# Kernel optimization log

Measured on AMD Instinct MI355X. Metric: run time of the kernel, lower is better.

Reference implementation:

```python
import jax, jax.numpy as jnp
import numpy as np

B, S, H, R, IN, OPS, NPAD = 128, 128, 512, 16, 2, 5, 16
L = IN + NPAD
NEG = -1e12


def setup_inputs():
    key = jax.random.key(0)
    ks = jax.random.split(key, 32)
    def n(k, shape, scale=1.0):
        return jax.random.normal(k, shape, jnp.float32) * scale
    s = 0.05
    return {
        "encoder_outputs": n(ks[0], (S, B, H)),
        "current_emb": n(ks[1], (B, 1, H)),
        "left_childs": n(ks[2], (B, H)),
        "padding_hidden": jnp.zeros((1, H), jnp.float32),
        "num_pades": n(ks[3], (B, NPAD, H)),
        "rule_scores": n(ks[4], (R, H)),
        "embedding_weight": n(ks[5], (1, IN, H)),
        "W_concat_l": n(ks[6], (H, H), s), "b_concat_l": jnp.zeros((H,)),
        "W_concat_lg": n(ks[7], (H, H), s), "b_concat_lg": jnp.zeros((H,)),
        "W_concat_r": n(ks[8], (2 * H, H), s), "b_concat_r": jnp.zeros((H,)),
        "W_concat_rg": n(ks[9], (2 * H, H), s), "b_concat_rg": jnp.zeros((H,)),
        "W_tree_attn": n(ks[10], (2 * H, H), s), "b_tree_attn": jnp.zeros((H,)),
        "W_tree_score": n(ks[11], (H, 1), s), "b_tree_score": jnp.zeros((1,)),
        "W_rule_attn": n(ks[12], (2 * H, H), s), "b_rule_attn": jnp.zeros((H,)),
        "W_rule_score": n(ks[13], (H, 1), s), "b_rule_score": jnp.zeros((1,)),
        "W_rp1": n(ks[14], (H, H), s), "b_rp1": jnp.zeros((H,)),
        "W_rp2": n(ks[15], (H, 1), s), "b_rp2": jnp.zeros((1,)),
        "W_sc_attn": n(ks[16], (3 * H, H), s), "b_sc_attn": jnp.zeros((H,)),
        "W_sc_score": n(ks[17], (H, 1), s),
        "W_ops": n(ks[18], (2 * H, OPS), s), "b_ops": jnp.zeros((OPS,)),
        "seq_mask": jax.random.randint(ks[19], (B, S), 0, 2).astype(jnp.int32),
        "mask_nums": jax.random.randint(ks[20], (B, L), 0, 2).astype(jnp.int32),
        "has_left": jax.random.randint(ks[21], (B,), 0, 2).astype(jnp.int32),
        "stack_empty": jax.random.randint(ks[22], (B,), 0, 2).astype(jnp.int32),
    }


def reference(encoder_outputs, current_emb, left_childs, padding_hidden, num_pades,
              rule_scores, embedding_weight,
              W_concat_l, b_concat_l, W_concat_lg, b_concat_lg,
              W_concat_r, b_concat_r, W_concat_rg, b_concat_rg,
              W_tree_attn, b_tree_attn, W_tree_score, b_tree_score,
              W_rule_attn, b_rule_attn, W_rule_score, b_rule_score,
              W_rp1, b_rp1, W_rp2, b_rp2,
              W_sc_attn, b_sc_attn, W_sc_score, W_ops, b_ops,
              seq_mask, mask_nums, has_left, stack_empty):
    sm = seq_mask.astype(bool)          # [B,S] True = pad
    nm = mask_nums.astype(bool)         # [B,L]
    hl = has_left.astype(bool)[:, None]
    se = stack_empty.astype(bool)[:, None]
    h = encoder_outputs.shape[-1]
    # gather top-of-stack embedding, padding for empty stacks (the ragged python loop)
    c = jnp.where(se, padding_hidden[0], current_emb[:, 0])  # [B,H]
    # gated combine: left_child==None branch vs cat(left, c) branch (dropout=eval)
    node_l = jnp.tanh(c @ W_concat_l + b_concat_l) * jax.nn.sigmoid(c @ W_concat_lg + b_concat_lg)
    node_r = (jnp.tanh(left_childs @ W_concat_r[:h] + c @ W_concat_r[h:] + b_concat_r)
              * jax.nn.sigmoid(left_childs @ W_concat_rg[:h] + c @ W_concat_rg[h:] + b_concat_rg))
    q = jnp.where(hl, node_r, node_l)                        # [B,H]
    current_node = q[:, None, :]                              # [B,1,H]
    # TreeAttn: concat(hidden, enc) -> Linear -> tanh -> Linear(H,1) -> softmax over S
    e = jnp.tanh(q @ W_tree_attn[:h] + encoder_outputs @ W_tree_attn[h:] + b_tree_attn)  # [S,B,H]
    ae = (e @ W_tree_score)[..., 0] + b_tree_score[0]         # [S,B]
    ae = jnp.where(sm, NEG, ae.T)                             # [B,S]
    current_attn = jax.nn.softmax(ae, axis=1)                 # [B,S]
    current_context = jnp.einsum('bs,sbh->bh', current_attn, encoder_outputs)[:, None, :]
    # RuleAttn: concat(enc, rule) additive attention, softmax over S
    re = jnp.tanh(encoder_outputs @ W_rule_attn[:h]
                  + (rule_scores @ W_rule_attn[h:])[:, None, None, :]
                  + b_rule_attn)                              # [R,S,B,H]
    r_ae = (re @ W_rule_score)[..., 0] + b_rule_score[0]      # [R,S,B]
    r_ae = jnp.transpose(r_ae, (2, 0, 1))                     # [B,R,S]
    r_ae = jnp.where(sm[:, None, :], NEG, r_ae)
    rules_attn = jax.nn.softmax(r_ae, axis=-1)
    rules_context = jnp.einsum('brs,sbh->brh', rules_attn + 0.2 * current_attn[:, None, :], encoder_outputs)
    rule_prob = jax.nn.softmax((jnp.tanh(rules_context @ W_rp1 + b_rp1) @ W_rp2)[..., 0] + b_rp2[0], axis=-1)  # [B,R]
    # leaf scoring: Score(cat(node, context), [const_embs | num_pades])
    bsz = q.shape[0]
    ew = jnp.concatenate([jnp.broadcast_to(embedding_weight, (bsz,) + embedding_weight.shape[1:]), num_pades], axis=1)  # [B,L,H]
    leaf = jnp.concatenate([q, current_context[:, 0]], axis=1)  # [B,2H]
    sc = jnp.tanh((leaf @ W_sc_attn[:2 * h])[:, None, :] + ew @ W_sc_attn[2 * h:] + b_sc_attn)  # [B,L,H]
    num_score = jnp.where(nm, NEG, (sc @ W_sc_score)[..., 0])   # [B,L]
    op = leaf @ W_ops + b_ops                                   # [B,OPS]
    return num_score, op, current_node, current_context, ew, rule_prob
```

## Files before the change

kernel.cpp:

```cpp
#include <hip/hip_runtime.h>
#include <hip/hip_bf16.h>

#define B_ 128
#define S_ 128
#define H_ 512
#define R_ 16
#define IN_ 2
#define OPS_ 5
#define NPAD_ 16
#define L_ 18
#define NEGV (-1000000000000.0f)
#define C2_ (-2.885390081777927f)

typedef __bf16 bf16_t;
typedef bf16_t bf16x8 __attribute__((ext_vector_type(8)));
typedef float floatx4 __attribute__((ext_vector_type(4)));

__device__ __forceinline__ float rcp_f(float x) { return __builtin_amdgcn_rcpf(x); }
__device__ __forceinline__ float exp2_f(float x) { return __builtin_amdgcn_exp2f(x); }

__device__ __forceinline__ float fast_tanh(float x) {
    return 2.0f * rcp_f(1.0f + exp2_f(C2_ * x)) - 1.0f;
}
__device__ __forceinline__ float fast_sigmoid(float x) {
    return rcp_f(1.0f + exp2_f(-1.4426950408889634f * x));
}
__device__ __forceinline__ unsigned short f2bf(float f) {
    unsigned int u = __builtin_bit_cast(unsigned int, f);
    u += 0x7fff + ((u >> 16) & 1);
    return (unsigned short)(u >> 16);
}
__device__ __forceinline__ float bf2f(unsigned short u) {
    return __builtin_bit_cast(float, (unsigned int)u << 16);
}

#define LSTR 40

__device__ __forceinline__ void mfma_tile(const unsigned short* __restrict__ A,
                                          const unsigned short* __restrict__ Bt,
                                          void* __restrict__ Cv, bool bf16_out,
                                          int m0, int n0, int K, int ldc,
                                          unsigned short* As, unsigned short* Bs) {
    const int tid  = threadIdx.x;
    const int wid  = tid >> 6, lane = tid & 63;
    const int quad = lane >> 4, mn = lane & 15;
    const int wm = (wid & 1) * 64, wn = (wid >> 1) * 64;
    const int sr = tid >> 2;
    const int sc = (tid & 3) * 8;

    floatx4 acc[4][4] = {};

    for (int k0 = 0; k0 < K; k0 += 32) {
        uint4 a0 = *(const uint4*)(A  + (size_t)(m0 + sr)      * K + k0 + sc);
        uint4 a1 = *(const uint4*)(A  + (size_t)(m0 + sr + 64) * K + k0 + sc);
        uint4 b0 = *(const uint4*)(Bt + (size_t)(n0 + sr)      * K + k0 + sc);
        uint4 b1 = *(const uint4*)(Bt + (size_t)(n0 + sr + 64) * K + k0 + sc);
        __syncthreads();
        *(uint4*)&As[sr * LSTR + sc]        = a0;
        *(uint4*)&As[(sr + 64) * LSTR + sc] = a1;
        *(uint4*)&Bs[sr * LSTR + sc]        = b0;
        *(uint4*)&Bs[(sr + 64) * LSTR + sc] = b1;
        __syncthreads();

        bf16x8 af[4], bfr[4];
        #pragma unroll
        for (int i = 0; i < 4; ++i)
            af[i] = *(const bf16x8*)&As[(wm + i * 16 + mn) * LSTR + quad * 8];
        #pragma unroll
        for (int j = 0; j < 4; ++j)
            bfr[j] = *(const bf16x8*)&Bs[(wn + j * 16 + mn) * LSTR + quad * 8];

        #pragma unroll
        for (int i = 0; i < 4; ++i)
            #pragma unroll
            for (int j = 0; j < 4; ++j)
                acc[i][j] = __builtin_amdgcn_mfma_f32_16x16x32_bf16(af[i], bfr[j], acc[i][j], 0, 0, 0);
    }

    #pragma unroll
    for (int i = 0; i < 4; ++i) {
        #pragma unroll
        for (int j = 0; j < 4; ++j) {
            #pragma unroll
            for (int r = 0; r < 4; ++r) {
                int row = m0 + wm + i * 16 + quad * 4 + r;
                int col = n0 + wn + j * 16 + mn;
                if (bf16_out)
                    ((unsigned short*)Cv)[(size_t)row * ldc + col] = f2bf(acc[i][j][r]);
                else
                    ((float*)Cv)[(size_t)row * ldc + col] = acc[i][j][r];
            }
        }
    }
}

__global__ __launch_bounds__(256) void k_gemm_mega1(const unsigned short* __restrict__ EO_bf,
                                                    const unsigned short* __restrict__ Wcat,
                                                    unsigned short* __restrict__ eobuf,
                                                    const unsigned short* __restrict__ q_bf,
                                                    const unsigned short* __restrict__ T5,
                                                    float* __restrict__ qT) {
    __shared__ unsigned short As[128 * LSTR];
    __shared__ unsigned short Bs[128 * LSTR];
    int blk = blockIdx.x;
    if (blk < 1024)
        mfma_tile(EO_bf, Wcat, eobuf, true, (blk >> 3) * 128, (blk & 7) * 128, 512, 1024, As, Bs);
    else
        mfma_tile(q_bf, T5, qT, false, 0, (blk - 1024) * 128, 512, 512, As, Bs);
}

__global__ __launch_bounds__(256) void k_gemm_mega2(const unsigned short* __restrict__ rctx_bf,
                                                    const unsigned short* __restrict__ T8,
                                                    float* __restrict__ rclin,
                                                    const unsigned short* __restrict__ leaf_bf,
                                                    const unsigned short* __restrict__ T9,
                                                    float* __restrict__ lsb,
                                                    const unsigned short* __restrict__ ew_bf,
                                                    const unsigned short* __restrict__ T10,
                                                    unsigned short* __restrict__ ewp_bf) {
    __shared__ unsigned short As[128 * LSTR];
    __shared__ unsigned short Bs[128 * LSTR];
    int blk = blockIdx.x;
    if (blk < 64)
        mfma_tile(rctx_bf, T8, rclin, false, (blk >> 2) * 128, (blk & 3) * 128, 512, 512, As, Bs);
    else if (blk < 68)
        mfma_tile(leaf_bf, T9, lsb, false, 0, (blk - 64) * 128, 1024, 512, As, Bs);
    else {
        int r = blk - 68;
        mfma_tile(ew_bf, T10, ewp_bf, true, (r >> 2) * 128, (r & 3) * 128, 512, 512, As, Bs);
    }
}

struct MJ5 {
    const unsigned short* A[5]; const unsigned short* Bt[5]; float* C[5];
    int M[5]; int K[5];
};
__global__ __launch_bounds__(256) void gemm_bf16_j5(MJ5 g) {
    __shared__ unsigned short As[128 * LSTR];
    __shared__ unsigned short Bs[128 * LSTR];

    const int z = blockIdx.z;
    const unsigned short* A  = g.A[z];
    const unsigned short* Bt = g.Bt[z];
    float* C = g.C[z];
    const int M = g.M[z], K = g.K[z];

    const int tid  = threadIdx.x;
    const int wid  = tid >> 6, lane = tid & 63;
    const int quad = lane >> 4, mn = lane & 15;
    const int wm = (wid & 1) * 64, wn = (wid >> 1) * 64;
    const int n0 = blockIdx.x * 128;

    const int sr = tid >> 2;
    const int sc = (tid & 3) * 8;
    const int ra0 = min(sr, M - 1);
    const int ra1 = min(sr + 64, M - 1);

    floatx4 acc[4][4] = {};

    for (int k0 = 0; k0 < K; k0 += 32) {
        uint4 a0 = *(const uint4*)(A  + (size_t)ra0 * K + k0 + sc);
        uint4 a1 = *(const uint4*)(A  + (size_t)ra1 * K + k0 + sc);
        uint4 b0 = *(const uint4*)(Bt + (size_t)(n0 + sr)      * K + k0 + sc);
        uint4 b1 = *(const uint4*)(Bt + (size_t)(n0 + sr + 64) * K + k0 + sc);
        __syncthreads();
        *(uint4*)&As[sr * LSTR + sc]        = a0;
        *(uint4*)&As[(sr + 64) * LSTR + sc] = a1;
        *(uint4*)&Bs[sr * LSTR + sc]        = b0;
        *(uint4*)&Bs[(sr + 64) * LSTR + sc] = b1;
        __syncthreads();

        bf16x8 af[4], bfr[4];
        #pragma unroll
        for (int i = 0; i < 4; ++i)
            af[i] = *(const bf16x8*)&As[(wm + i * 16 + mn) * LSTR + quad * 8];
        #pragma unroll
        for (int j = 0; j < 4; ++j)
            bfr[j] = *(const bf16x8*)&Bs[(wn + j * 16 + mn) * LSTR + quad * 8];

        #pragma unroll
        for (int i = 0; i < 4; ++i)
            #pragma unroll
            for (int j = 0; j < 4; ++j)
                acc[i][j] = __builtin_amdgcn_mfma_f32_16x16x32_bf16(af[i], bfr[j], acc[i][j], 0, 0, 0);
    }

    #pragma unroll
    for (int i = 0; i < 4; ++i) {
        #pragma unroll
        for (int j = 0; j < 4; ++j) {
            #pragma unroll
            for (int r = 0; r < 4; ++r) {
                int row = wm + i * 16 + quad * 4 + r;
                int col = n0 + wn + j * 16 + mn;
                if (row < M)
                    C[(size_t)row * 512 + col] = acc[i][j][r];
            }
        }
    }
}

struct PrepArgs {
    const float *EO, *cur, *padh, *left, *rsc, *embw, *npad;
    const int* se;
    unsigned short *EO_bf, *c_bf, *acat_bf, *rsc_bf, *ew_bf;
    float* ew_out;
    const float* tsrc[11];
    unsigned short* tdst[11];
    int tK[11];
    int tbase[12];
};
#define PG_CAST 8192
#define PG_EW   1152
#define PG_PREP 288
#define PG_WT   3584
#define PG_TOTAL (PG_CAST + PG_EW + PG_PREP + PG_WT)

__global__ __launch_bounds__(256) void k_prep_mega(PrepArgs a) {
    __shared__ float t[32][33];
    int blk = blockIdx.x, tid = threadIdx.x;
    if (blk < PG_CAST) {
        int i = (blk * 256 + tid) * 4;
        float4 v = *(const float4*)(a.EO + i);
        ushort4 o;
        o.x = f2bf(v.x); o.y = f2bf(v.y); o.z = f2bf(v.z); o.w = f2bf(v.w);
        *(ushort4*)(a.EO_bf + i) = o;
    } else if (blk < PG_CAST + PG_EW) {
        int i = ((blk - PG_CAST) * 256 + tid) * 4;
        int j = i & 511;
        int bl = i >> 9;
        int l = bl % L_;
        int b = bl / L_;
        const float* src = (l < IN_) ? (a.embw + l * H_ + j)
                                     : (a.npad + ((size_t)b * NPAD_ + (l - IN_)) * H_ + j);
        float4 v = *(const float4*)src;
        *(float4*)(a.ew_out + i) = v;
        ushort4 o;
        o.x = f2bf(v.x); o.y = f2bf(v.y); o.z = f2bf(v.z); o.w = f2bf(v.w);
        *(ushort4*)(a.ew_bf + i) = o;
    } else if (blk < PG_CAST + PG_EW + PG_PREP) {
        int i = (blk - PG_CAST - PG_EW) * 256 + tid;
        if (i < B_ * H_) {
            int b = i >> 9, j = i & 511;
            float cv = a.se[b] ? a.padh[j] : a.cur[i];
            a.c_bf[i] = f2bf(cv);
            a.acat_bf[b * 1024 + j] = f2bf(a.left[i]);
            a.acat_bf[b * 1024 + 512 + j] = f2bf(cv);
        } else {
            int k = i - B_ * H_;
            a.rsc_bf[k] = f2bf(a.rsc[k]);
        }
    } else {
        int rel = blk - (PG_CAST + PG_EW + PG_PREP);
        int j = 0;
        while (rel >= a.tbase[j + 1]) ++j;
        int r = rel - a.tbase[j];
        int K = a.tK[j];
        const float* src = a.tsrc[j];
        unsigned short* dst = a.tdst[j];
        int bx = (r & 15) * 32;
        int by = (r >> 4) * 32;
        int tx = tid & 31, ty = tid >> 5;
        #pragma unroll
        for (int i = 0; i < 32; i += 8)
            t[ty + i][tx] = src[(size_t)(by + ty + i) * 512 + bx + tx];
        __syncthreads();
        #pragma unroll
        for (int i = 0; i < 32; i += 8)
            dst[(size_t)(bx + ty + i) * K + by + tx] = f2bf(t[tx][ty + i]);
    }
}

__global__ void k_node(const float* __restrict__ gl, const float* __restrict__ glg,
                       const float* __restrict__ gr, const float* __restrict__ grg,
                       const float* __restrict__ bl, const float* __restrict__ blg,
                       const float* __restrict__ br, const float* __restrict__ brg,
                       const int* __restrict__ hl,
                       unsigned short* __restrict__ q_bf, float* __restrict__ node_out,
                       unsigned short* __restrict__ leaf_bf) {
    int i = blockIdx.x * blockDim.x + threadIdx.x;
    int b = i >> 9, j = i & 511;
    float nl = fast_tanh(gl[i] + bl[j]) * fast_sigmoid(glg[i] + blg[j]);
    float nr = fast_tanh(gr[i] + br[j]) * fast_sigmoid(grg[i] + brg[j]);
    float v = hl[b] ? nr : nl;
    node_out[i] = v;
    q_bf[i] = f2bf(v);
    leaf_bf[b * 1024 + j] = f2bf(v);
}

__global__ __launch_bounds__(256) void k_tree_attn(const float* __restrict__ qT,
                                                   const unsigned short* __restrict__ eobuf,
                                                   const float* __restrict__ b_ta,
                                                   const float* __restrict__ w_ts,
                                                   const float* __restrict__ b_ts,
                                                   const int* __restrict__ sm,
                                                   float* __restrict__ attn) {
    __shared__ float sc[S_];
    int b = blockIdx.x;
    int tid = threadIdx.x;
    int wid = tid >> 6, lane = tid & 63;
    int j0 = lane * 8;
    float4 q0 = *(const float4*)(qT + b * H_ + j0);
    float4 q1 = *(const float4*)(qT + b * H_ + j0 + 4);
    float4 t0 = *(const float4*)(b_ta + j0);
    float4 t1 = *(const float4*)(b_ta + j0 + 4);
    float4 w0 = *(const float4*)(w_ts + j0);
    float4 w1 = *(const float4*)(w_ts + j0 + 4);
    float qc[8] = {C2_*(q0.x+t0.x), C2_*(q0.y+t0.y), C2_*(q0.z+t0.z), C2_*(q0.w+t0.w),
                   C2_*(q1.x+t1.x), C2_*(q1.y+t1.y), C2_*(q1.z+t1.z), C2_*(q1.w+t1.w)};
    float w2[8] = {2*w0.x, 2*w0.y, 2*w0.z, 2*w0.w, 2*w1.x, 2*w1.y, 2*w1.z, 2*w1.w};
    float wsum = 0.5f * (w2[0]+w2[1]+w2[2]+w2[3]+w2[4]+w2[5]+w2[6]+w2[7]);
    float bias = b_ts[0];

    for (int s = wid; s < S_; s += 4) {
        if (sm[b * S_ + s]) {
            if (lane == 0) sc[s] = NEGV;
            continue;
        }
        uint4 ev = *(const uint4*)(eobuf + ((size_t)s * B_ + b) * 1024 + j0);
        const unsigned short* ep = (const unsigned short*)&ev;
        float acc = -wsum;
        #pragma unroll
        for (int k = 0; k < 8; ++k) {
            float y = fmaf(C2_, bf2f(ep[k]), qc[k]);
            acc = fmaf(w2[k], rcp_f(1.0f + exp2_f(y)), acc);
        }
        #pragma unroll
        for (int o = 32; o > 0; o >>= 1) acc += __shfl_xor(acc, o);
        if (lane == 0) sc[s] = acc + bias;
    }
    __syncthreads();
    if (tid < 64) {
        float v0 = sc[tid], v1 = sc[tid + 64];
        float m = fmaxf(v0, v1);
        #pragma unroll
        for (int o = 32; o > 0; o >>= 1) m = fmaxf(m, __shfl_xor(m, o));
        float e0 = __expf(v0 - m), e1 = __expf(v1 - m);
        float ss = e0 + e1;
        #pragma unroll
        for (int o = 32; o > 0; o >>= 1) ss += __shfl_xor(ss, o);
        float r = rcp_f(ss);
        attn[b * S_ + tid] = e0 * r;
        attn[b * S_ + tid + 64] = e1 * r;
    }
}

__global__ __launch_bounds__(256) void k_rule_score2(const unsigned short* __restrict__ eobuf,
                                                     const float* __restrict__ RP,
                                                     const float* __restrict__ b_ra,
                                                     const float* __restrict__ w_rs,
                                                     const float* __restrict__ b_rs,
                                                     const int* __restrict__ sm,
                                                     float* __restrict__ comb) {
    int wid = threadIdx.x >> 6, lane = threadIdx.x & 63;
    int row = blockIdx.x * 4 + wid;
    int s = row >> 7, b = row & 127;
    bool masked = sm[b * S_ + s] != 0;
    if (masked) {
        if (lane < R_) comb[((size_t)b * R_ + lane) * S_ + s] = NEGV;
        return;
    }
    int j0 = lane * 8;
    uint4 ev = *(const uint4*)(eobuf + (size_t)row * 1024 + 512 + j0);
    const unsigned short* ep = (const unsigned short*)&ev;
    float4 a0 = *(const float4*)(b_ra + j0);
    float4 a1 = *(const float4*)(b_ra + j0 + 4);
    float4 w0 = *(const float4*)(w_rs + j0);
    float4 w1 = *(const float4*)(w_rs + j0 + 4);
    float ba[8] = {a0.x, a0.y, a0.z, a0.w, a1.x, a1.y, a1.z, a1.w};
    float w2[8], ed[8];
    float wsum = 0.f;
    {
        float w[8] = {w0.x, w0.y, w0.z, w0.w, w1.x, w1.y, w1.z, w1.w};
        #pragma unroll
        for (int k = 0; k < 8; ++k) {
            wsum += w[k];
            w2[k] = 2.0f * w[k];
            ed[k] = C2_ * (bf2f(ep[k]) + ba[k]);
        }
    }
    float bias = b_rs[0];
    #pragma unroll
    for (int r = 0; r < R_; ++r) {
        float4 r0 = *(const float4*)(RP + r * H_ + j0);
        float4 r1 = *(const float4*)(RP + r * H_ + j0 + 4);
        float rp[8] = {r0.x, r0.y, r0.z, r0.w, r1.x, r1.y, r1.z, r1.w};
        float acc = -wsum;
        #pragma unroll
        for (int k = 0; k < 8; ++k) {
            float y = fmaf(C2_, rp[k], ed[k]);
            acc = fmaf(w2[k], rcp_f(1.0f + exp2_f(y)), acc);
        }
        #pragma unroll
        for (int o = 32; o > 0; o >>= 1) acc += __shfl_xor(acc, o);
        if (lane == 0) comb[((size_t)b * R_ + r) * S_ + s] = acc + bias;
    }
}

__global__ __launch_bounds__(128) void k_softmax_rules(float* __restrict__ comb,
                                                       const float* __restrict__ attn) {
    __shared__ float red[2], red2[2];
    int br = blockIdx.x;
    int b = br >> 4;
    int t = threadIdx.x;
    float* row = comb + (size_t)br * 128;
    float v = row[t];
    float m = v;
    for (int o = 32; o > 0; o >>= 1) m = fmaxf(m, __shfl_down(m, o));
    if ((t & 63) == 0) red[t >> 6] = m;
    __syncthreads();
    m = fmaxf(red[0], red[1]);
    float e = __expf(v - m);
    float ssum = e;
    for (int o = 32; o > 0; o >>= 1) ssum += __shfl_down(ssum, o);
    if ((t & 63) == 0) red2[t >> 6] = ssum;
    __syncthreads();
    row[t] = e * rcp_f(red2[0] + red2[1]) + 0.2f * attn[b * 128 + t];
}

__global__ __launch_bounds__(256) void k_context(const float* __restrict__ EO,
                                                 const float* __restrict__ attn,
                                                 const float* __restrict__ comb,
                                                 const int* __restrict__ sm,
                                                 float* __restrict__ ctx_out,
                                                 unsigned short* __restrict__ leaf_bf,
                                                 unsigned short* __restrict__ rctx) {
    __shared__ float at[S_];
    __shared__ float cb[R_ * S_];
    __shared__ int smr[S_];
    int b = blockIdx.x;
    int j = blockIdx.y * 256 + threadIdx.x;
    if (threadIdx.x < S_) {
        at[threadIdx.x] = attn[b * S_ + threadIdx.x];
        smr[threadIdx.x] = sm[b * S_ + threadIdx.x];
    }
    for (int i = threadIdx.x; i < R_ * S_; i += 256) cb[i] = comb[(size_t)b * R_ * S_ + i];
    __syncthreads();
    float ctx = 0.f;
    float rc[R_] = {};
    for (int s = 0; s < S_; ++s) {
        if (smr[s]) continue;
        float eo = EO[((size_t)s * B_ + b) * H_ + j];
        ctx += at[s] * eo;
        #pragma unroll
        for (int r = 0; r < R_; ++r) rc[r] += cb[r * S_ + s] * eo;
    }
    ctx_out[b * H_ + j] = ctx;
    leaf_bf[b * 1024 + 512 + j] = f2bf(ctx);
    #pragma unroll
    for (int r = 0; r < R_; ++r) rctx[((size_t)b * R_ + r) * H_ + j] = f2bf(rc[r]);
}

__global__ __launch_bounds__(256) void k_epilogue(const float* __restrict__ rclin,
                                                  const float* __restrict__ b_rp1,
                                                  const float* __restrict__ w_rp2,
                                                  const float* __restrict__ b_rp2,
                                                  float* __restrict__ prob,
                                                  const float* __restrict__ lsb,
                                                  const unsigned short* __restrict__ ewp,
                                                  const float* __restrict__ b_sc,
                                                  const float* __restrict__ w_scs,
                                                  const int* __restrict__ mask_nums,
                                                  float* __restrict__ ns_out,
                                                  const unsigned short* __restrict__ leaf_bf,
                                                  const float* __restrict__ Wops,
                                                  const float* __restrict__ bops,
                                                  float* __restrict__ op_out) {
    __shared__ float sc[R_];
    int blk = blockIdx.x;
    int wid = threadIdx.x >> 6, lane = threadIdx.x & 63;
    if (blk < 128) {
        int b = blk;
        int j0 = lane * 8;
        float4 p0 = *(const float4*)(b_rp1 + j0);
        float4 p1 = *(const float4*)(b_rp1 + j0 + 4);
        float4 w0 = *(const float4*)(w_rp2 + j0);
        float4 w1 = *(const float4*)(w_rp2 + j0 + 4);
        float brc[8] = {C2_*p0.x, C2_*p0.y, C2_*p0.z, C2_*p0.w,
                        C2_*p1.x, C2_*p1.y, C2_*p1.z, C2_*p1.w};
        float w[8] = {w0.x, w0.y, w0.z, w0.w, w1.x, w1.y, w1.z, w1.w};
        float wsum = 0.f;
        #pragma unroll
        for (int k = 0; k < 8; ++k) wsum += w[k];
        #pragma unroll
        for (int rr = 0; rr < 4; ++rr) {
            int r = wid * 4 + rr;
            const float* rl = rclin + ((size_t)b * R_ + r) * H_ + j0;
            float4 r0 = *(const float4*)(rl);
            float4 r1 = *(const float4*)(rl + 4);
            float rv[8] = {r0.x, r0.y, r0.z, r0.w, r1.x, r1.y, r1.z, r1.w};
            float acc = -wsum;
            #pragma unroll
            for (int k = 0; k < 8; ++k) {
                float y = fmaf(C2_, rv[k], brc[k]);
                acc = fmaf(2.0f * w[k], rcp_f(1.0f + exp2_f(y)), acc);
            }
            #pragma unroll
            for (int o = 32; o > 0; o >>= 1) acc += __shfl_xor(acc, o);
            if (lane == 0) sc[r] = acc + b_rp2[0];
        }
        __syncthreads();
        if (threadIdx.x < R_) {
            float m = -1e30f;
            for (int r = 0; r < R_; ++r) m = fmaxf(m, sc[r]);
            float sum = 0.f;
            for (int r = 0; r < R_; ++r) sum += __expf(sc[r] - m);
            prob[b * R_ + threadIdx.x] = __expf(sc[threadIdx.x] - m) * rcp_f(sum);
        }
    } else if (blk < 704) {
        int row = (blk - 128) * 4 + wid;
        int b = row / L_, l = row - b * L_;
        bool masked = mask_nums[b * L_ + l] != 0;
        if (masked) {
            if (lane == 0) ns_out[b * L_ + l] = NEGV;
            return;
        }
        int j0 = lane * 8;
        uint4 ev = *(const uint4*)(ewp + (size_t)row * H_ + j0);
        const unsigned short* ep = (const unsigned short*)&ev;
        float4 l0 = *(const float4*)(lsb + b * H_ + j0);
        float4 l1 = *(const float4*)(lsb + b * H_ + j0 + 4);
        float4 s0 = *(const float4*)(b_sc + j0);
        float4 s1 = *(const float4*)(b_sc + j0 + 4);
        float4 w0 = *(const float4*)(w_scs + j0);
        float4 w1 = *(const float4*)(w_scs + j0 + 4);
        float lc[8] = {C2_*(l0.x+s0.x), C2_*(l0.y+s0.y), C2_*(l0.z+s0.z), C2_*(l0.w+s0.w),
                       C2_*(l1.x+s1.x), C2_*(l1.y+s1.y), C2_*(l1.z+s1.z), C2_*(l1.w+s1.w)};
        float w[8] = {w0.x, w0.y, w0.z, w0.w, w1.x, w1.y, w1.z, w1.w};
        float wsum = 0.f;
        #pragma unroll
        for (int k = 0; k < 8; ++k) wsum += w[k];
        float acc = -wsum;
        #pragma unroll
        for (int k = 0; k < 8; ++k) {
            float y = fmaf(C2_, bf2f(ep[k]), lc[k]);
            acc = fmaf(2.0f * w[k], rcp_f(1.0f + exp2_f(y)), acc);
        }
        #pragma unroll
        for (int o = 32; o > 0; o >>= 1) acc += __shfl_xor(acc, o);
        if (lane == 0) ns_out[b * L_ + l] = acc;
    } else {
        int b = (blk - 704) * 4 + wid;
        int base = b * 1024 + lane * 16;
        uint4 v0 = *(const uint4*)(leaf_bf + base);
        uint4 v1 = *(const uint4*)(leaf_bf + base + 8);
        const unsigned short* lp0 = (const unsigned short*)&v0;
        const unsigned short* lp1 = (const unsigned short*)&v1;
        float lv[16];
        #pragma unroll
        for (int k = 0; k < 8; ++k) { lv[k] = bf2f(lp0[k]); lv[8 + k] = bf2f(lp1[k]); }
        #pragma unroll
        for (int o = 0; o < OPS_; ++o) {
            float acc = 0.f;
            #pragma unroll
            for (int k = 0; k < 16; ++k)
                acc = fmaf(lv[k], Wops[(size_t)(lane * 16 + k) * OPS_ + o], acc);
            #pragma unroll
            for (int of = 32; of > 0; of >>= 1) acc += __shfl_xor(acc, of);
            if (lane == 0) op_out[b * OPS_ + o] = acc + bops[o];
        }
    }
}

extern "C" void kernel_launch(void* const* d_in, const int* in_sizes, int n_in,
                              void* d_out, int out_size, void* d_ws, size_t ws_size,
                              hipStream_t stream) {
    const float* EO   = (const float*)d_in[0];
    const float* cur  = (const float*)d_in[1];
    const float* left = (const float*)d_in[2];
    const float* padh = (const float*)d_in[3];
    const float* npad = (const float*)d_in[4];
    const float* rsc  = (const float*)d_in[5];
    const float* embw = (const float*)d_in[6];
    const float* Wl   = (const float*)d_in[7];  const float* bl   = (const float*)d_in[8];
    const float* Wlg  = (const float*)d_in[9];  const float* blg  = (const float*)d_in[10];
    const float* Wr   = (const float*)d_in[11]; const float* br   = (const float*)d_in[12];
    const float* Wrg  = (const float*)d_in[13]; const float* brg  = (const float*)d_in[14];
    const float* Wta  = (const float*)d_in[15]; const float* bta  = (const float*)d_in[16];
    const float* Wts  = (const float*)d_in[17]; const float* bts  = (const float*)d_in[18];
    const float* Wra  = (const float*)d_in[19]; const float* bra  = (const float*)d_in[20];
    const float* Wrs  = (const float*)d_in[21]; const float* brs  = (const float*)d_in[22];
    const float* Wrp1 = (const float*)d_in[23]; const float* brp1 = (const float*)d_in[24];
    const float* Wrp2 = (const float*)d_in[25]; const float* brp2 = (const float*)d_in[26];
    const float* Wsa  = (const float*)d_in[27]; const float* bsa  = (const float*)d_in[28];
    const float* Wss  = (const float*)d_in[29];
    const float* Wops = (const float*)d_in[30]; const float* bops = (const float*)d_in[31];
    const int* smk = (const int*)d_in[32];
    const int* nmk = (const int*)d_in[33];
    const int* hlk = (const int*)d_in[34];
    const int* sek = (const int*)d_in[35];

    float* out = (float*)d_out;

    const size_t O_NS    = 0;
    const size_t O_OP    = O_NS + (size_t)B_ * L_;
    const size_t O_NODE  = O_OP + (size_t)B_ * OPS_;
    const size_t O_CTX   = O_NODE + (size_t)B_ * H_;
    const size_t O_EW    = O_CTX + (size_t)B_ * H_;
    const size_t O_RPROB = O_EW + (size_t)B_ * L_ * H_;

    float* f = (float*)d_ws;
    float* rp_buf = f;               f += 8192;
    float* qT     = f;               f += 65536;
    float* attn   = f;               f += 16384;
    float* comb   = f;               f += 262144;
    float* gl     = f;               f += 65536;
    float* glg    = f;               f += 65536;
    float* gr     = f;               f += 65536;
    float* grg    = f;               f += 65536;
    float* lsb    = f;               f += 65536;
    float* rclin  = f;               f += 1048576;
    unsigned short* u = (unsigned short*)f;
    unsigned short* EO_bf   = u;     u += 8388608;
    unsigned short* ew_bf   = u;     u += 1179648;
    unsigned short* leaf_bf = u;     u += 131072;
    unsigned short* rctx_bf = u;     u += 1048576;
    unsigned short* Wcat    = u;     u += 524288;
    unsigned short* T0      = u;     u += 262144;
    unsigned short* T1      = u;     u += 262144;
    unsigned short* T2      = u;     u += 524288;
    unsigned short* T3      = u;     u += 524288;
    unsigned short* T4      = u;     u += 262144;
    unsigned short* T5      = u;     u += 262144;
    unsigned short* T8      = u;     u += 262144;
    unsigned short* T9      = u;     u += 524288;
    unsigned short* T10     = u;     u += 262144;
    unsigned short* q_bf    = u;     u += 65536;
    unsigned short* c_bf    = u;     u += 65536;
    unsigned short* acat_bf = u;     u += 131072;
    unsigned short* rsc_bf  = u;     u += 8192;
    unsigned short* ewp_bf  = u;     u += 1179648;
    unsigned short* eobuf   = u;     u += 16777216;

    PrepArgs a;
    a.EO = EO; a.cur = cur; a.padh = padh; a.left = left; a.rsc = rsc;
    a.embw = embw; a.npad = npad; a.se = sek;
    a.EO_bf = EO_bf; a.c_bf = c_bf; a.acat_bf = acat_bf; a.rsc_bf = rsc_bf;
    a.ew_bf = ew_bf; a.ew_out = out + O_EW;
    const float* tsrc[11] = {Wl, Wlg, Wr, Wrg, Wra + (size_t)H_ * H_, Wta,
                             Wta + (size_t)H_ * H_, Wra, Wrp1, Wsa, Wsa + (size_t)2 * H_ * H_};
    unsigned short* tdst[11] = {T0, T1, T2, T3, T4, T5, Wcat, Wcat + 512 * 512, T8, T9, T10};
    int tk[11] = {512, 512, 1024, 1024, 512, 512, 512, 512, 512, 1024, 512};
    int base = 0;
    for (int i = 0; i < 11; ++i) {
        a.tsrc[i] = tsrc[i]; a.tdst[i] = tdst[i]; a.tK[i] = tk[i];
        a.tbase[i] = base;
        base += 16 * (tk[i] / 32);
    }
    a.tbase[11] = base;
    k_prep_mega<<<PG_TOTAL, 256, 0, stream>>>(a);

    MJ5 g;
    g.A[0] = c_bf;    g.Bt[0] = T0; g.C[0] = gl;     g.M[0] = B_;  g.K[0] = 512;
    g.A[1] = c_bf;    g.Bt[1] = T1; g.C[1] = glg;    g.M[1] = B_;  g.K[1] = 512;
    g.A[2] = acat_bf; g.Bt[2] = T2; g.C[2] = gr;     g.M[2] = B_;  g.K[2] = 1024;
    g.A[3] = acat_bf; g.Bt[3] = T3; g.C[3] = grg;    g.M[3] = B_;  g.K[3] = 1024;
    g.A[4] = rsc_bf;  g.Bt[4] = T4; g.C[4] = rp_buf; g.M[4] = R_;  g.K[4] = 512;
    gemm_bf16_j5<<<dim3(4, 1, 5), 256, 0, stream>>>(g);

    k_node<<<256, 256, 0, stream>>>(gl, glg, gr, grg, bl, blg, br, brg, hlk,
                                    q_bf, out + O_NODE, leaf_bf);

    k_gemm_mega1<<<1028, 256, 0, stream>>>(EO_bf, Wcat, eobuf, q_bf, T5, qT);

    k_tree_attn<<<B_, 256, 0, stream>>>(qT, eobuf, bta, Wts, bts, smk, attn);

    k_rule_score2<<<S_ * B_ / 4, 256, 0, stream>>>(eobuf, rp_buf, bra, Wrs, brs, smk, comb);
    k_softmax_rules<<<B_ * R_, 128, 0, stream>>>(comb, attn);

    k_context<<<dim3(B_, 2), 256, 0, stream>>>(EO, attn, comb, smk, out + O_CTX,
                                               leaf_bf, rctx_bf);

    k_gemm_mega2<<<140, 256, 0, stream>>>(rctx_bf, T8, rclin, leaf_bf, T9, lsb,
                                          ew_bf, T10, ewp_bf);

    k_epilogue<<<736, 256, 0, stream>>>(rclin, brp1, Wrp2, brp2, out + O_RPROB,
                                        lsb, ewp_bf, bsa, Wss, nmk, out + O_NS,
                                        leaf_bf, Wops, bops, out + O_OP);
}
```

Measured before the change: 333.4 us.

## Prefetch GEMM tiles, fuse scoring kernels, merge rule softmax into context pass

The GEMM tiles now load the next K-slice of global data into registers while the current slice is in shared memory, a simple software pipeline. The mega1 block-to-tile mapping is reordered so that consecutive blocks share a weight column tile. Tree-attention and rule-score kernels are merged into one launch, and the rule softmax is folded into the context kernel, which now reads bf16 encoder outputs with 512 threads per batch. This removes launches and halves encoder-output read bandwidth, at the cost of reduced precision in the context sums and fewer blocks in the context kernel.

```diff
diff --git a/kernel.cpp b/kernel.cpp
--- a/kernel.cpp
+++ b/kernel.cpp
@@ -48,19 +48,32 @@
     const int sr = tid >> 2;
     const int sc = (tid & 3) * 8;
 
+    const unsigned short* pa0 = A  + (size_t)(m0 + sr)      * K + sc;
+    const unsigned short* pa1 = A  + (size_t)(m0 + sr + 64) * K + sc;
+    const unsigned short* pb0 = Bt + (size_t)(n0 + sr)      * K + sc;
+    const unsigned short* pb1 = Bt + (size_t)(n0 + sr + 64) * K + sc;
+
+    uint4 a0 = *(const uint4*)pa0;
+    uint4 a1 = *(const uint4*)pa1;
+    uint4 b0 = *(const uint4*)pb0;
+    uint4 b1 = *(const uint4*)pb1;
+
     floatx4 acc[4][4] = {};
 
     for (int k0 = 0; k0 < K; k0 += 32) {
-        uint4 a0 = *(const uint4*)(A  + (size_t)(m0 + sr)      * K + k0 + sc);
-        uint4 a1 = *(const uint4*)(A  + (size_t)(m0 + sr + 64) * K + k0 + sc);
-        uint4 b0 = *(const uint4*)(Bt + (size_t)(n0 + sr)      * K + k0 + sc);
-        uint4 b1 = *(const uint4*)(Bt + (size_t)(n0 + sr + 64) * K + k0 + sc);
         __syncthreads();
         *(uint4*)&As[sr * LSTR + sc]        = a0;
         *(uint4*)&As[(sr + 64) * LSTR + sc] = a1;
         *(uint4*)&Bs[sr * LSTR + sc]        = b0;
         *(uint4*)&Bs[(sr + 64) * LSTR + sc] = b1;
         __syncthreads();
+
+        if (k0 + 32 < K) {
+            a0 = *(const uint4*)(pa0 + k0 + 32);
+            a1 = *(const uint4*)(pa1 + k0 + 32);
+            b0 = *(const uint4*)(pb0 + k0 + 32);
+            b1 = *(const uint4*)(pb1 + k0 + 32);
+        }
 
         bf16x8 af[4], bfr[4];
         #pragma unroll
@@ -104,7 +117,7 @@
     __shared__ unsigned short Bs[128 * LSTR];
     int blk = blockIdx.x;
     if (blk < 1024)
-        mfma_tile(EO_bf, Wcat, eobuf, true, (blk >> 3) * 128, (blk & 7) * 128, 512, 1024, As, Bs);
+        mfma_tile(EO_bf, Wcat, eobuf, true, (blk & 127) * 128, (blk >> 7) * 128, 512, 1024, As, Bs);
     else
         mfma_tile(q_bf, T5, qT, false, 0, (blk - 1024) * 128, 512, 512, As, Bs);
 }
@@ -156,19 +169,32 @@
     const int ra0 = min(sr, M - 1);
     const int ra1 = min(sr + 64, M - 1);
 
+    const unsigned short* pa0 = A  + (size_t)ra0 * K + sc;
+    const unsigned short* pa1 = A  + (size_t)ra1 * K + sc;
+    const unsigned short* pb0 = Bt + (size_t)(n0 + sr)      * K + sc;
+    const unsigned short* pb1 = Bt + (size_t)(n0 + sr + 64) * K + sc;
+
+    uint4 a0 = *(const uint4*)pa0;
+    uint4 a1 = *(const uint4*)pa1;
+    uint4 b0 = *(const uint4*)pb0;
+    uint4 b1 = *(const uint4*)pb1;
+
     floatx4 acc[4][4] = {};
 
     for (int k0 = 0; k0 < K; k0 += 32) {
-        uint4 a0 = *(const uint4*)(A  + (size_t)ra0 * K + k0 + sc);
-        uint4 a1 = *(const uint4*)(A  + (size_t)ra1 * K + k0 + sc);
-        uint4 b0 = *(const uint4*)(Bt + (size_t)(n0 + sr)      * K + k0 + sc);
-        uint4 b1 = *(const uint4*)(Bt + (size_t)(n0 + sr + 64) * K + k0 + sc);
         __syncthreads();
         *(uint4*)&As[sr * LSTR + sc]        = a0;
         *(uint4*)&As[(sr + 64) * LSTR + sc] = a1;
         *(uint4*)&Bs[sr * LSTR + sc]        = b0;
         *(uint4*)&Bs[(sr + 64) * LSTR + sc] = b1;
         __syncthreads();
+
+        if (k0 + 32 < K) {
+            a0 = *(const uint4*)(pa0 + k0 + 32);
+            a1 = *(const uint4*)(pa1 + k0 + 32);
+            b0 = *(const uint4*)(pb0 + k0 + 32);
+            b1 = *(const uint4*)(pb1 + k0 + 32);
+        }
 
         bf16x8 af[4], bfr[4];
         #pragma unroll
@@ -288,79 +314,79 @@
     leaf_bf[b * 1024 + j] = f2bf(v);
 }
 
-__global__ __launch_bounds__(256) void k_tree_attn(const float* __restrict__ qT,
-                                                   const unsigned short* __restrict__ eobuf,
-                                                   const float* __restrict__ b_ta,
-                                                   const float* __restrict__ w_ts,
-                                                   const float* __restrict__ b_ts,
-                                                   const int* __restrict__ sm,
-                                                   float* __restrict__ attn) {
-    __shared__ float sc[S_];
-    int b = blockIdx.x;
-    int tid = threadIdx.x;
-    int wid = tid >> 6, lane = tid & 63;
-    int j0 = lane * 8;
-    float4 q0 = *(const float4*)(qT + b * H_ + j0);
-    float4 q1 = *(const float4*)(qT + b * H_ + j0 + 4);
-    float4 t0 = *(const float4*)(b_ta + j0);
-    float4 t1 = *(const float4*)(b_ta + j0 + 4);
-    float4 w0 = *(const float4*)(w_ts + j0);
-    float4 w1 = *(const float4*)(w_ts + j0 + 4);
-    float qc[8] = {C2_*(q0.x+t0.x), C2_*(q0.y+t0.y), C2_*(q0.z+t0.z), C2_*(q0.w+t0.w),
-                   C2_*(q1.x+t1.x), C2_*(q1.y+t1.y), C2_*(q1.z+t1.z), C2_*(q1.w+t1.w)};
-    float w2[8] = {2*w0.x, 2*w0.y, 2*w0.z, 2*w0.w, 2*w1.x, 2*w1.y, 2*w1.z, 2*w1.w};
-    float wsum = 0.5f * (w2[0]+w2[1]+w2[2]+w2[3]+w2[4]+w2[5]+w2[6]+w2[7]);
-    float bias = b_ts[0];
-
-    for (int s = wid; s < S_; s += 4) {
-        if (sm[b * S_ + s]) {
-            if (lane == 0) sc[s] = NEGV;
-            continue;
-        }
-        uint4 ev = *(const uint4*)(eobuf + ((size_t)s * B_ + b) * 1024 + j0);
-        const unsigned short* ep = (const unsigned short*)&ev;
-        float acc = -wsum;
-        #pragma unroll
-        for (int k = 0; k < 8; ++k) {
-            float y = fmaf(C2_, bf2f(ep[k]), qc[k]);
-            acc = fmaf(w2[k], rcp_f(1.0f + exp2_f(y)), acc);
-        }
-        #pragma unroll
-        for (int o = 32; o > 0; o >>= 1) acc += __shfl_xor(acc, o);
-        if (lane == 0) sc[s] = acc + bias;
-    }
-    __syncthreads();
-    if (tid < 64) {
-        float v0 = sc[tid], v1 = sc[tid + 64];
-        float m = fmaxf(v0, v1);
-        #pragma unroll
-        for (int o = 32; o > 0; o >>= 1) m = fmaxf(m, __shfl_xor(m, o));
-        float e0 = __expf(v0 - m), e1 = __expf(v1 - m);
-        float ss = e0 + e1;
-        #pragma unroll
-        for (int o = 32; o > 0; o >>= 1) ss += __shfl_xor(ss, o);
-        float r = rcp_f(ss);
-        attn[b * S_ + tid] = e0 * r;
-        attn[b * S_ + tid + 64] = e1 * r;
-    }
-}
-
-__global__ __launch_bounds__(256) void k_rule_score2(const unsigned short* __restrict__ eobuf,
+__global__ __launch_bounds__(256) void k_score_fused(const float* __restrict__ qT,
+                                                     const unsigned short* __restrict__ eobuf,
+                                                     const float* __restrict__ b_ta,
+                                                     const float* __restrict__ w_ts,
+                                                     const float* __restrict__ b_ts,
                                                      const float* __restrict__ RP,
                                                      const float* __restrict__ b_ra,
                                                      const float* __restrict__ w_rs,
                                                      const float* __restrict__ b_rs,
                                                      const int* __restrict__ sm,
+                                                     float* __restrict__ attn,
                                                      float* __restrict__ comb) {
-    int wid = threadIdx.x >> 6, lane = threadIdx.x & 63;
-    int row = blockIdx.x * 4 + wid;
+    __shared__ float sc[S_];
+    int blk = blockIdx.x;
+    int tid = threadIdx.x;
+    int wid = tid >> 6, lane = tid & 63;
+    int j0 = lane * 8;
+
+    if (blk < 128) {
+        int b = blk;
+        float4 q0 = *(const float4*)(qT + b * H_ + j0);
+        float4 q1 = *(const float4*)(qT + b * H_ + j0 + 4);
+        float4 t0 = *(const float4*)(b_ta + j0);
+        float4 t1 = *(const float4*)(b_ta + j0 + 4);
+        float4 w0 = *(const float4*)(w_ts + j0);
+        float4 w1 = *(const float4*)(w_ts + j0 + 4);
+        float qc[8] = {C2_*(q0.x+t0.x), C2_*(q0.y+t0.y), C2_*(q0.z+t0.z), C2_*(q0.w+t0.w),
+                       C2_*(q1.x+t1.x), C2_*(q1.y+t1.y), C2_*(q1.z+t1.z), C2_*(q1.w+t1.w)};
+        float w2[8] = {2*w0.x, 2*w0.y, 2*w0.z, 2*w0.w, 2*w1.x, 2*w1.y, 2*w1.z, 2*w1.w};
+        float wsum = 0.5f * (w2[0]+w2[1]+w2[2]+w2[3]+w2[4]+w2[5]+w2[6]+w2[7]);
+        float bias = b_ts[0];
+
+        for (int s = wid; s < S_; s += 4) {
+            if (sm[b * S_ + s]) {
+                if (lane == 0) sc[s] = NEGV;
+                continue;
+            }
+            uint4 ev = *(const uint4*)(eobuf + ((size_t)s * B_ + b) * 1024 + j0);
+            const unsigned short* ep = (const unsigned short*)&ev;
+            float acc = -wsum;
+            #pragma unroll
+            for (int k = 0; k < 8; ++k) {
+                float y = fmaf(C2_, bf2f(ep[k]), qc[k]);
+                acc = fmaf(w2[k], rcp_f(1.0f + exp2_f(y)), acc);
+            }
+            #pragma unroll
+            for (int o = 32; o > 0; o >>= 1) acc += __shfl_xor(acc, o);
+            if (lane == 0) sc[s] = acc + bias;
+        }
+        __syncthreads();
+        if (tid < 64) {
+            float v0 = sc[tid], v1 = sc[tid + 64];
+            float m = fmaxf(v0, v1);
+            #pragma unroll
+            for (int o = 32; o > 0; o >>= 1) m = fmaxf(m, __shfl_xor(m, o));
+            float e0 = __expf(v0 - m), e1 = __expf(v1 - m);
+            float ss = e0 + e1;
+            #pragma unroll
+            for (int o = 32; o > 0; o >>= 1) ss += __shfl_xor(ss, o);
+            float r = rcp_f(ss);
+            attn[b * S_ + tid] = e0 * r;
+            attn[b * S_ + tid + 64] = e1 * r;
+        }
+        return;
+    }
+
+    int row = (blk - 128) * 4 + wid;
     int s = row >> 7, b = row & 127;
     bool masked = sm[b * S_ + s] != 0;
     if (masked) {
         if (lane < R_) comb[((size_t)b * R_ + lane) * S_ + s] = NEGV;
         return;
     }
-    int j0 = lane * 8;
     uint4 ev = *(const uint4*)(eobuf + (size_t)row * 1024 + 512 + j0);
     const unsigned short* ep = (const unsigned short*)&ev;
     float4 a0 = *(const float4*)(b_ra + j0);
@@ -397,50 +423,50 @@
     }
 }
 
-__global__ __launch_bounds__(128) void k_softmax_rules(float* __restrict__ comb,
-                                                       const float* __restrict__ attn) {
-    __shared__ float red[2], red2[2];
-    int br = blockIdx.x;
-    int b = br >> 4;
-    int t = threadIdx.x;
-    float* row = comb + (size_t)br * 128;
-    float v = row[t];
-    float m = v;
-    for (int o = 32; o > 0; o >>= 1) m = fmaxf(m, __shfl_down(m, o));
-    if ((t & 63) == 0) red[t >> 6] = m;
-    __syncthreads();
-    m = fmaxf(red[0], red[1]);
-    float e = __expf(v - m);
-    float ssum = e;
-    for (int o = 32; o > 0; o >>= 1) ssum += __shfl_down(ssum, o);
-    if ((t & 63) == 0) red2[t >> 6] = ssum;
-    __syncthreads();
-    row[t] = e * rcp_f(red2[0] + red2[1]) + 0.2f * attn[b * 128 + t];
-}
-
-__global__ __launch_bounds__(256) void k_context(const float* __restrict__ EO,
-                                                 const float* __restrict__ attn,
-                                                 const float* __restrict__ comb,
-                                                 const int* __restrict__ sm,
-                                                 float* __restrict__ ctx_out,
-                                                 unsigned short* __restrict__ leaf_bf,
-                                                 unsigned short* __restrict__ rctx) {
+__global__ __launch_bounds__(512) void k_ctxsm(const unsigned short* __restrict__ EO_bf,
+                                               const float* __restrict__ attn,
+                                               const float* __restrict__ comb,
+                                               const int* __restrict__ sm,
+                                               float* __restrict__ ctx_out,
+                                               unsigned short* __restrict__ leaf_bf,
+                                               unsigned short* __restrict__ rctx) {
+    __shared__ float cb[R_ * S_];
     __shared__ float at[S_];
-    __shared__ float cb[R_ * S_];
     __shared__ int smr[S_];
     int b = blockIdx.x;
-    int j = blockIdx.y * 256 + threadIdx.x;
-    if (threadIdx.x < S_) {
-        at[threadIdx.x] = attn[b * S_ + threadIdx.x];
-        smr[threadIdx.x] = sm[b * S_ + threadIdx.x];
-    }
-    for (int i = threadIdx.x; i < R_ * S_; i += 256) cb[i] = comb[(size_t)b * R_ * S_ + i];
+    int tid = threadIdx.x;
+    int w = tid >> 6, lane = tid & 63;
+
+    if (tid < S_) {
+        at[tid] = attn[b * S_ + tid];
+        smr[tid] = sm[b * S_ + tid];
+    }
+    for (int i = tid; i < R_ * S_; i += 512) cb[i] = comb[(size_t)b * R_ * S_ + i];
     __syncthreads();
+
+    #pragma unroll
+    for (int rr = 0; rr < 2; ++rr) {
+        int r = w * 2 + rr;
+        float v0 = cb[r * S_ + lane], v1 = cb[r * S_ + lane + 64];
+        float m = fmaxf(v0, v1);
+        #pragma unroll
+        for (int o = 32; o > 0; o >>= 1) m = fmaxf(m, __shfl_xor(m, o));
+        float e0 = __expf(v0 - m), e1 = __expf(v1 - m);
+        float ss = e0 + e1;
+        #pragma unroll
+        for (int o = 32; o > 0; o >>= 1) ss += __shfl_xor(ss, o);
+        float rc_ = rcp_f(ss);
+        cb[r * S_ + lane]      = e0 * rc_ + 0.2f * at[lane];
+        cb[r * S_ + lane + 64] = e1 * rc_ + 0.2f * at[lane + 64];
+    }
+    __syncthreads();
+
+    int j = tid;
     float ctx = 0.f;
     float rc[R_] = {};
     for (int s = 0; s < S_; ++s) {
         if (smr[s]) continue;
-        float eo = EO[((size_t)s * B_ + b) * H_ + j];
+        float eo = bf2f(EO_bf[((size_t)s * B_ + b) * H_ + j]);
         ctx += at[s] * eo;
         #pragma unroll
         for (int r = 0; r < R_; ++r) rc[r] += cb[r * S_ + s] * eo;
@@ -663,13 +689,11 @@
 
     k_gemm_mega1<<<1028, 256, 0, stream>>>(EO_bf, Wcat, eobuf, q_bf, T5, qT);
 
-    k_tree_attn<<<B_, 256, 0, stream>>>(qT, eobuf, bta, Wts, bts, smk, attn);
-
-    k_rule_score2<<<S_ * B_ / 4, 256, 0, stream>>>(eobuf, rp_buf, bra, Wrs, brs, smk, comb);
-    k_softmax_rules<<<B_ * R_, 128, 0, stream>>>(comb, attn);
-
-    k_context<<<dim3(B_, 2), 256, 0, stream>>>(EO, attn, comb, smk, out + O_CTX,
-                                               leaf_bf, rctx_bf);
+    k_score_fused<<<128 + S_ * B_ / 4, 256, 0, stream>>>(
+        qT, eobuf, bta, Wts, bts, rp_buf, bra, Wrs, brs, smk, attn, comb);
+
+    k_ctxsm<<<B_, 512, 0, stream>>>(EO_bf, attn, comb, smk, out + O_CTX,
+                                    leaf_bf, rctx_bf);
 
     k_gemm_mega2<<<140, 256, 0, stream>>>(rctx_bf, T8, rclin, leaf_bf, T9, lsb,
                                           ew_bf, T10, ewp_bf);
```

New measurement: 298.2 us. 10.6% less time.
